# Kernel optimization log

Measured on AMD Instinct MI355X. Metric: run time of the kernel, lower is better.

The kernel has to match this reference:

```python
import jax, jax.numpy as jnp
import numpy as np

ATT_DEPTH = 3
PATCH = 8


def setup_inputs() -> dict:
    key = jax.random.key(0)
    k1, k2 = jax.random.split(key)
    B, C, H, W = 8, 16, 512, 512
    x = jax.random.normal(k1, (B, C, H, W), dtype=jnp.float32)
    L = (H // PATCH) * (W // PATCH)            # 4096 target patches
    Lp = (H // (PATCH * 2 ** ATT_DEPTH)) * (W // (PATCH * 2 ** ATT_DEPTH))  # 64 source patches
    attentions = jax.random.uniform(k2, (B, 1, L, Lp), dtype=jnp.float32)
    return {"x": x, "attentions": attentions}


def reference(x, attentions):
    B, C, H, W = x.shape
    d = 2 ** ATT_DEPTH
    p = PATCH
    # depthwise ones-conv stride d, divided by d*d == average pooling
    argx = x.reshape(B, C, H // d, d, W // d, d).mean(axis=(3, 5))  # [B,C,h,w]
    h, w = H // d, W // d
    hp, wp = h // p, w // p
    # nn.Unfold(kernel=p, stride=p): channels ordered (C, kh, kw), locations row-major
    unf = (argx.reshape(B, C, hp, p, wp, p)
               .transpose(0, 1, 3, 5, 2, 4)
               .reshape(B, C * p * p, hp * wp))  # [B, C*p*p, L']
    # normalize attention rows by nonzero count (non-differentiable int count)
    nz = jax.lax.stop_gradient(
        jnp.count_nonzero(attentions, axis=-1).astype(attentions.dtype)
    )[..., None] + 1e-05  # [B,1,L,1]
    # [B,1,L,L'] @ [B,1,L',C*p*p] -> [B,1,L,C*p*p]
    att = jnp.matmul(attentions / nz, unf[:, None].transpose(0, 1, 3, 2))
    att = jnp.squeeze(att, axis=1).transpose(0, 2, 1)  # [B, C*p*p, L]
    # Fold(output=(H,W), kernel=p, stride=p): non-overlapping -> pure reshape
    Hp, Wp = H // p, W // p
    out = (att.reshape(B, C, p, p, Hp, Wp)
              .transpose(0, 1, 4, 2, 5, 3)
              .reshape(B, C, H, W))
    return out
```

## Files before the change

kernel.cpp:

```cpp
#include <hip/hip_runtime.h>
#include <hip/hip_bf16.h>

typedef __attribute__((ext_vector_type(4))) float f32x4;
typedef __attribute__((ext_vector_type(8))) short s16x8;

#define NB 8
#define NC 16
#define HH 512
#define WW 512

__global__ __launch_bounds__(256) void pool_to_bt(const float* __restrict__ x,
                                                  __hip_bfloat16* __restrict__ bt) {
    int flat = blockIdx.x * 256 + threadIdx.x;
    int wq = flat & 63;
    int hq = (flat >> 6) & 63;
    int c  = (flat >> 12) & 15;
    int b  = flat >> 16;
    const float* base = x + ((size_t)(b * NC + c) * HH + hq * 8) * WW + wq * 8;
    float s = 0.f;
#pragma unroll
    for (int r = 0; r < 8; ++r) {
        f32x4 v0 = *(const f32x4*)(base + (size_t)r * WW);
        f32x4 v1 = *(const f32x4*)(base + (size_t)r * WW + 4);
        s += v0[0] + v0[1] + v0[2] + v0[3] + v1[0] + v1[1] + v1[2] + v1[3];
    }
    s *= (1.f / 64.f);
    int m  = c * 64 + (hq & 7) * 8 + (wq & 7);
    int lp = (hq >> 3) * 8 + (wq >> 3);
    bt[((size_t)b * 1024 + m) * 64 + lp] = __float2bfloat16(s);
}

#define BM 128
#define BN 128
#define LDK 72

__global__ __launch_bounds__(256) void gemm_scatter(const float* __restrict__ attn,
                                                    const __hip_bfloat16* __restrict__ bt,
                                                    float* __restrict__ out) {
    int mb = blockIdx.x;
    int lb = blockIdx.y;
    int b  = blockIdx.z;

    __shared__ __align__(16) unsigned short As[BM][LDK];
    __shared__ __align__(16) unsigned short Bs[BN][LDK];

    int tid = threadIdx.x;

    {
        int row  = tid >> 1;
        int half = tid & 1;
        const float* Arow = attn + ((size_t)(b * 4096 + lb * BM + row)) * 64 + half * 32;
        f32x4 v[8];
        int cnt = 0;
#pragma unroll
        for (int j = 0; j < 8; ++j) {
            v[j] = *(const f32x4*)(Arow + j * 4);
            cnt += (v[j][0] != 0.f) + (v[j][1] != 0.f) + (v[j][2] != 0.f) + (v[j][3] != 0.f);
        }
        cnt += __shfl_xor(cnt, 1);
        float inv = 1.0f / ((float)cnt + 1e-5f);
#pragma unroll
        for (int j = 0; j < 4; ++j) {
            s16x8 o;
#pragma unroll
            for (int e = 0; e < 8; ++e) {
                __hip_bfloat16 h = __float2bfloat16(v[j * 2 + (e >> 2)][e & 3] * inv);
                o[e] = (short)*reinterpret_cast<unsigned short*>(&h);
            }
            *(s16x8*)&As[row][half * 32 + j * 8] = o;
        }
    }
    {
        const unsigned short* Bg = (const unsigned short*)bt + ((size_t)b * 1024 + mb * BN) * 64;
#pragma unroll
        for (int i = 0; i < 4; ++i) {
            int cid = tid + i * 256;
            int row = cid >> 3, c8 = cid & 7;
            *(s16x8*)&Bs[row][c8 * 8] = *(const s16x8*)(Bg + row * 64 + c8 * 8);
        }
    }
    __syncthreads();

    int w    = tid >> 6;
    int lane = tid & 63;
    int wm   = (w & 1) * 64;
    int wl   = (w >> 1) * 64;
    int lr   = lane & 15;
    int kq   = lane >> 4;

    f32x4 acc[4][4] = {};
#pragma unroll
    for (int ks = 0; ks < 2; ++ks) {
        s16x8 mf[4], lf[4];
#pragma unroll
        for (int i = 0; i < 4; ++i)
            mf[i] = *(const s16x8*)&Bs[wm + i * 16 + lr][ks * 32 + kq * 8];
#pragma unroll
        for (int j = 0; j < 4; ++j)
            lf[j] = *(const s16x8*)&As[wl + j * 16 + lr][ks * 32 + kq * 8];
#pragma unroll
        for (int i = 0; i < 4; ++i)
#pragma unroll
            for (int j = 0; j < 4; ++j)
                acc[i][j] = __builtin_amdgcn_mfma_f32_16x16x32_bf16(mf[i], lf[j], acc[i][j], 0, 0, 0);
    }

#pragma unroll
    for (int mi = 0; mi < 4; ++mi) {
        int m0 = mb * BN + wm + mi * 16 + kq * 4;
        int c  = m0 >> 6, kh = (m0 >> 3) & 7, kw = m0 & 7;
        float* obase = out + (((size_t)(b * NC + c) * HH) + kh) * WW + kw;
#pragma unroll
        for (int lj = 0; lj < 4; ++lj) {
            int l  = lb * BM + wl + lj * 16 + lr;
            int Hp = l >> 6, Wp = l & 63;
            *(f32x4*)(obase + ((size_t)Hp * 8) * WW + Wp * 8) = acc[mi][lj];
        }
    }
}

extern "C" void kernel_launch(void* const* d_in, const int* in_sizes, int n_in,
                              void* d_out, int out_size, void* d_ws, size_t ws_size,
                              hipStream_t stream) {
    const float* x    = (const float*)d_in[0];
    const float* attn = (const float*)d_in[1];
    float* out        = (float*)d_out;

    __hip_bfloat16* bt = (__hip_bfloat16*)d_ws;

    pool_to_bt<<<2048, 256, 0, stream>>>(x, bt);
    dim3 grid(8, 32, 8);
    gemm_scatter<<<grid, 256, 0, stream>>>(attn, bt, out);
}
```

Before: 56.75 us.

## Use nontemporal loads/stores, coalesce attention loads, and remap gemm block order

Loads of x in the pooling kernel and output stores in the gemm kernel become nontemporal, so streaming data bypasses cache retention. The attention tile load is restructured so 16 consecutive threads read one 64-float row with coalesced 16-byte accesses, and the nonzero count is reduced with four xor shuffles. The grid becomes 1D with batch as the fastest index and the M-block as the slowest, which changes which blocks run concurrently and how they share cache. The trade-off is more shuffle instructions per row and narrower 8-byte LDS writes.

```diff
diff --git a/kernel.cpp b/kernel.cpp
--- a/kernel.cpp
+++ b/kernel.cpp
@@ -2,6 +2,7 @@
 #include <hip/hip_bf16.h>
 
 typedef __attribute__((ext_vector_type(4))) float f32x4;
+typedef __attribute__((ext_vector_type(4))) short s16x4;
 typedef __attribute__((ext_vector_type(8))) short s16x8;
 
 #define NB 8
@@ -20,8 +21,8 @@
     float s = 0.f;
 #pragma unroll
     for (int r = 0; r < 8; ++r) {
-        f32x4 v0 = *(const f32x4*)(base + (size_t)r * WW);
-        f32x4 v1 = *(const f32x4*)(base + (size_t)r * WW + 4);
+        f32x4 v0 = __builtin_nontemporal_load((const f32x4*)(base + (size_t)r * WW));
+        f32x4 v1 = __builtin_nontemporal_load((const f32x4*)(base + (size_t)r * WW + 4));
         s += v0[0] + v0[1] + v0[2] + v0[3] + v1[0] + v1[1] + v1[2] + v1[3];
     }
     s *= (1.f / 64.f);
@@ -37,9 +38,10 @@
 __global__ __launch_bounds__(256) void gemm_scatter(const float* __restrict__ attn,
                                                     const __hip_bfloat16* __restrict__ bt,
                                                     float* __restrict__ out) {
-    int mb = blockIdx.x;
-    int lb = blockIdx.y;
-    int b  = blockIdx.z;
+    int bi = blockIdx.x;
+    int mb = bi >> 8;
+    int lb = (bi >> 3) & 31;
+    int b  = bi & 7;
 
     __shared__ __align__(16) unsigned short As[BM][LDK];
     __shared__ __align__(16) unsigned short Bs[BN][LDK];
@@ -47,27 +49,26 @@
     int tid = threadIdx.x;
 
     {
-        int row  = tid >> 1;
-        int half = tid & 1;
-        const float* Arow = attn + ((size_t)(b * 4096 + lb * BM + row)) * 64 + half * 32;
-        f32x4 v[8];
-        int cnt = 0;
+        const float* Abase = attn + ((size_t)(b * 4096 + lb * BM)) * 64;
 #pragma unroll
-        for (int j = 0; j < 8; ++j) {
-            v[j] = *(const f32x4*)(Arow + j * 4);
-            cnt += (v[j][0] != 0.f) + (v[j][1] != 0.f) + (v[j][2] != 0.f) + (v[j][3] != 0.f);
-        }
-        cnt += __shfl_xor(cnt, 1);
-        float inv = 1.0f / ((float)cnt + 1e-5f);
+        for (int i = 0; i < 8; ++i) {
+            int cid   = tid + i * 256;
+            int chunk = cid & 15;
+            int row   = cid >> 4;
+            f32x4 v = *(const f32x4*)(Abase + (size_t)row * 64 + chunk * 4);
+            int cnt = (v[0] != 0.f) + (v[1] != 0.f) + (v[2] != 0.f) + (v[3] != 0.f);
+            cnt += __shfl_xor(cnt, 1);
+            cnt += __shfl_xor(cnt, 2);
+            cnt += __shfl_xor(cnt, 4);
+            cnt += __shfl_xor(cnt, 8);
+            float inv = 1.0f / ((float)cnt + 1e-5f);
+            s16x4 o;
 #pragma unroll
-        for (int j = 0; j < 4; ++j) {
-            s16x8 o;
-#pragma unroll
-            for (int e = 0; e < 8; ++e) {
-                __hip_bfloat16 h = __float2bfloat16(v[j * 2 + (e >> 2)][e & 3] * inv);
+            for (int e = 0; e < 4; ++e) {
+                __hip_bfloat16 h = __float2bfloat16(v[e] * inv);
                 o[e] = (short)*reinterpret_cast<unsigned short*>(&h);
             }
-            *(s16x8*)&As[row][half * 32 + j * 8] = o;
+            *(s16x4*)&As[row][chunk * 4] = o;
         }
     }
     {
@@ -114,7 +115,8 @@
         for (int lj = 0; lj < 4; ++lj) {
             int l  = lb * BM + wl + lj * 16 + lr;
             int Hp = l >> 6, Wp = l & 63;
-            *(f32x4*)(obase + ((size_t)Hp * 8) * WW + Wp * 8) = acc[mi][lj];
+            __builtin_nontemporal_store(acc[mi][lj],
+                                        (f32x4*)(obase + ((size_t)Hp * 8) * WW + Wp * 8));
         }
     }
 }
@@ -129,6 +131,5 @@
     __hip_bfloat16* bt = (__hip_bfloat16*)d_ws;
 
     pool_to_bt<<<2048, 256, 0, stream>>>(x, bt);
-    dim3 grid(8, 32, 8);
-    gemm_scatter<<<grid, 256, 0, stream>>>(attn, bt, out);
+    gemm_scatter<<<2048, 256, 0, stream>>>(attn, bt, out);
 }
```

New measurement: 58.40 us. +2.9%, slower.

## Load GEMM fragments directly from global into registers, dropping LDS staging

Applied to the files above, without the earlier changes.

The GEMM kernel no longer stages A and B tiles through shared memory. Each wave loads its MFMA fragments straight from global memory, and the A rows are normalized in registers using a cross-lane shuffle count. This removes the LDS writes, LDS reads and the block barrier, and launch bounds now ask for 3 blocks per CU. In exchange each wave reloads data its sibling waves also fetch, which doubles redundant global and L2 traffic for A and B, and the per-lane global reads are strided.

```diff
diff --git a/kernel.cpp b/kernel.cpp
--- a/kernel.cpp
+++ b/kernel.cpp
@@ -30,57 +30,14 @@
     bt[((size_t)b * 1024 + m) * 64 + lp] = __float2bfloat16(s);
 }
 
-#define BM 128
-#define BN 128
-#define LDK 72
-
-__global__ __launch_bounds__(256) void gemm_scatter(const float* __restrict__ attn,
-                                                    const __hip_bfloat16* __restrict__ bt,
-                                                    float* __restrict__ out) {
+__global__ __launch_bounds__(256, 3) void gemm_scatter(const float* __restrict__ attn,
+                                                       const __hip_bfloat16* __restrict__ bt,
+                                                       float* __restrict__ out) {
     int mb = blockIdx.x;
     int lb = blockIdx.y;
     int b  = blockIdx.z;
 
-    __shared__ __align__(16) unsigned short As[BM][LDK];
-    __shared__ __align__(16) unsigned short Bs[BN][LDK];
-
-    int tid = threadIdx.x;
-
-    {
-        int row  = tid >> 1;
-        int half = tid & 1;
-        const float* Arow = attn + ((size_t)(b * 4096 + lb * BM + row)) * 64 + half * 32;
-        f32x4 v[8];
-        int cnt = 0;
-#pragma unroll
-        for (int j = 0; j < 8; ++j) {
-            v[j] = *(const f32x4*)(Arow + j * 4);
-            cnt += (v[j][0] != 0.f) + (v[j][1] != 0.f) + (v[j][2] != 0.f) + (v[j][3] != 0.f);
-        }
-        cnt += __shfl_xor(cnt, 1);
-        float inv = 1.0f / ((float)cnt + 1e-5f);
-#pragma unroll
-        for (int j = 0; j < 4; ++j) {
-            s16x8 o;
-#pragma unroll
-            for (int e = 0; e < 8; ++e) {
-                __hip_bfloat16 h = __float2bfloat16(v[j * 2 + (e >> 2)][e & 3] * inv);
-                o[e] = (short)*reinterpret_cast<unsigned short*>(&h);
-            }
-            *(s16x8*)&As[row][half * 32 + j * 8] = o;
-        }
-    }
-    {
-        const unsigned short* Bg = (const unsigned short*)bt + ((size_t)b * 1024 + mb * BN) * 64;
-#pragma unroll
-        for (int i = 0; i < 4; ++i) {
-            int cid = tid + i * 256;
-            int row = cid >> 3, c8 = cid & 7;
-            *(s16x8*)&Bs[row][c8 * 8] = *(const s16x8*)(Bg + row * 64 + c8 * 8);
-        }
-    }
-    __syncthreads();
-
+    int tid  = threadIdx.x;
     int w    = tid >> 6;
     int lane = tid & 63;
     int wm   = (w & 1) * 64;
@@ -88,31 +45,65 @@
     int lr   = lane & 15;
     int kq   = lane >> 4;
 
+    const unsigned short* Bg = (const unsigned short*)bt
+        + ((size_t)b * 1024 + mb * 128 + wm + lr) * 64 + kq * 8;
+    s16x8 mf[4][2];
+#pragma unroll
+    for (int i = 0; i < 4; ++i)
+#pragma unroll
+        for (int ks = 0; ks < 2; ++ks)
+            mf[i][ks] = *(const s16x8*)(Bg + (size_t)(i * 16) * 64 + ks * 32);
+
+    const float* Ag = attn + ((size_t)(b * 4096 + lb * 128 + wl + lr)) * 64 + kq * 8;
+    s16x8 lf[4][2];
+#pragma unroll
+    for (int j = 0; j < 4; ++j) {
+        f32x4 v[2][2];
+#pragma unroll
+        for (int ks = 0; ks < 2; ++ks) {
+            v[ks][0] = *(const f32x4*)(Ag + (size_t)(j * 16) * 64 + ks * 32);
+            v[ks][1] = *(const f32x4*)(Ag + (size_t)(j * 16) * 64 + ks * 32 + 4);
+        }
+        int cnt = 0;
+#pragma unroll
+        for (int ks = 0; ks < 2; ++ks)
+#pragma unroll
+            for (int h = 0; h < 2; ++h)
+                cnt += (v[ks][h][0] != 0.f) + (v[ks][h][1] != 0.f) +
+                       (v[ks][h][2] != 0.f) + (v[ks][h][3] != 0.f);
+        cnt += __shfl_xor(cnt, 16);
+        cnt += __shfl_xor(cnt, 32);
+        float inv = 1.0f / ((float)cnt + 1e-5f);
+#pragma unroll
+        for (int ks = 0; ks < 2; ++ks) {
+            s16x8 o;
+#pragma unroll
+            for (int e = 0; e < 8; ++e) {
+                __hip_bfloat16 h = __float2bfloat16(v[ks][e >> 2][e & 3] * inv);
+                o[e] = (short)*reinterpret_cast<unsigned short*>(&h);
+            }
+            lf[j][ks] = o;
+        }
+    }
+
     f32x4 acc[4][4] = {};
 #pragma unroll
-    for (int ks = 0; ks < 2; ++ks) {
-        s16x8 mf[4], lf[4];
-#pragma unroll
-        for (int i = 0; i < 4; ++i)
-            mf[i] = *(const s16x8*)&Bs[wm + i * 16 + lr][ks * 32 + kq * 8];
-#pragma unroll
-        for (int j = 0; j < 4; ++j)
-            lf[j] = *(const s16x8*)&As[wl + j * 16 + lr][ks * 32 + kq * 8];
+    for (int ks = 0; ks < 2; ++ks)
 #pragma unroll
         for (int i = 0; i < 4; ++i)
 #pragma unroll
             for (int j = 0; j < 4; ++j)
-                acc[i][j] = __builtin_amdgcn_mfma_f32_16x16x32_bf16(mf[i], lf[j], acc[i][j], 0, 0, 0);
-    }
+                acc[i][j] = __builtin_amdgcn_mfma_f32_16x16x32_bf16(mf[i][ks], lf[j][ks],
+                                                                    acc[i][j], 0, 0, 0);
 
 #pragma unroll
     for (int mi = 0; mi < 4; ++mi) {
-        int m0 = mb * BN + wm + mi * 16 + kq * 4;
+        int m0 = mb * 128 + wm + mi * 16 + kq * 4;
         int c  = m0 >> 6, kh = (m0 >> 3) & 7, kw = m0 & 7;
         float* obase = out + (((size_t)(b * NC + c) * HH) + kh) * WW + kw;
 #pragma unroll
         for (int lj = 0; lj < 4; ++lj) {
-            int l  = lb * BM + wl + lj * 16 + lr;
+            int l  = lb * 128 + wl + lj * 16 + lr;
             int Hp = l >> 6, Wp = l & 63;
             *(f32x4*)(obase + ((size_t)Hp * 8) * WW + Wp * 8) = acc[mi][lj];
         }
```

New measurement: 63.59 us. +12.1%, slower.

## Load B tile via global_load_lds with XOR-swizzled unpadded LDS layout

Applied to the files above, without the earlier changes.

Replaces the padded LDS tiles with unpadded 64-wide rows using an XOR swizzle on 16-byte chunks to avoid bank conflicts. The B tile now goes straight from global memory to LDS through global_load_lds instead of passing through registers. The B load is issued before the A conversion so the two overlap, and launch bounds request 5 blocks per CU. The aim is to cut LDS footprint and register traffic so occupancy can rise. The cost is more complex swizzle indexing that must match between writes and MFMA fragment reads.

```diff
diff --git a/kernel.cpp b/kernel.cpp
--- a/kernel.cpp
+++ b/kernel.cpp
@@ -30,26 +30,35 @@
     bt[((size_t)b * 1024 + m) * 64 + lp] = __float2bfloat16(s);
 }
 
-#define BM 128
-#define BN 128
-#define LDK 72
-
-__global__ __launch_bounds__(256) void gemm_scatter(const float* __restrict__ attn,
-                                                    const __hip_bfloat16* __restrict__ bt,
-                                                    float* __restrict__ out) {
+__global__ __launch_bounds__(256, 5) void gemm_scatter(const float* __restrict__ attn,
+                                                       const __hip_bfloat16* __restrict__ bt,
+                                                       float* __restrict__ out) {
     int mb = blockIdx.x;
     int lb = blockIdx.y;
     int b  = blockIdx.z;
 
-    __shared__ __align__(16) unsigned short As[BM][LDK];
-    __shared__ __align__(16) unsigned short Bs[BN][LDK];
+    __shared__ __align__(16) unsigned short As[128][64];
+    __shared__ __align__(16) unsigned short Bs[128][64];
 
     int tid = threadIdx.x;
 
     {
+        const unsigned short* Bg = (const unsigned short*)bt + ((size_t)b * 1024 + mb * 128) * 64;
+#pragma unroll
+        for (int i = 0; i < 4; ++i) {
+            int cid = tid + i * 256;
+            int row = cid >> 3, p = cid & 7;
+            const unsigned short* gsrc = Bg + row * 64 + (p ^ (row & 7)) * 8;
+            __builtin_amdgcn_global_load_lds(
+                (const __attribute__((address_space(1))) void*)gsrc,
+                (__attribute__((address_space(3))) void*)(&Bs[0][0] + (size_t)cid * 8),
+                16, 0, 0);
+        }
+    }
+    {
         int row  = tid >> 1;
         int half = tid & 1;
-        const float* Arow = attn + ((size_t)(b * 4096 + lb * BM + row)) * 64 + half * 32;
+        const float* Arow = attn + ((size_t)(b * 4096 + lb * 128 + row)) * 64 + half * 32;
         f32x4 v[8];
         int cnt = 0;
 #pragma unroll
@@ -67,16 +76,8 @@
                 __hip_bfloat16 h = __float2bfloat16(v[j * 2 + (e >> 2)][e & 3] * inv);
                 o[e] = (short)*reinterpret_cast<unsigned short*>(&h);
             }
-            *(s16x8*)&As[row][half * 32 + j * 8] = o;
-        }
-    }
-    {
-        const unsigned short* Bg = (const unsigned short*)bt + ((size_t)b * 1024 + mb * BN) * 64;
-#pragma unroll
-        for (int i = 0; i < 4; ++i) {
-            int cid = tid + i * 256;
-            int row = cid >> 3, c8 = cid & 7;
-            *(s16x8*)&Bs[row][c8 * 8] = *(const s16x8*)(Bg + row * 64 + c8 * 8);
+            int p = (half * 4 + j) ^ (row & 7);
+            *(s16x8*)&As[row][p * 8] = o;
         }
     }
     __syncthreads();
@@ -87,17 +88,19 @@
     int wl   = (w >> 1) * 64;
     int lr   = lane & 15;
     int kq   = lane >> 4;
+    int sw   = lr & 7;
 
     f32x4 acc[4][4] = {};
 #pragma unroll
     for (int ks = 0; ks < 2; ++ks) {
+        int p = (ks * 4 + kq) ^ sw;
         s16x8 mf[4], lf[4];
 #pragma unroll
         for (int i = 0; i < 4; ++i)
-            mf[i] = *(const s16x8*)&Bs[wm + i * 16 + lr][ks * 32 + kq * 8];
+            mf[i] = *(const s16x8*)&Bs[wm + i * 16 + lr][p * 8];
 #pragma unroll
         for (int j = 0; j < 4; ++j)
-            lf[j] = *(const s16x8*)&As[wl + j * 16 + lr][ks * 32 + kq * 8];
+            lf[j] = *(const s16x8*)&As[wl + j * 16 + lr][p * 8];
 #pragma unroll
         for (int i = 0; i < 4; ++i)
 #pragma unroll
@@ -107,12 +110,12 @@
 
 #pragma unroll
     for (int mi = 0; mi < 4; ++mi) {
-        int m0 = mb * BN + wm + mi * 16 + kq * 4;
+        int m0 = mb * 128 + wm + mi * 16 + kq * 4;
         int c  = m0 >> 6, kh = (m0 >> 3) & 7, kw = m0 & 7;
         float* obase = out + (((size_t)(b * NC + c) * HH) + kh) * WW + kw;
 #pragma unroll
         for (int lj = 0; lj < 4; ++lj) {
-            int l  = lb * BM + wl + lj * 16 + lr;
+            int l  = lb * 128 + wl + lj * 16 + lr;
             int Hp = l >> 6, Wp = l & 63;
             *(f32x4*)(obase + ((size_t)Hp * 8) * WW + Wp * 8) = acc[mi][lj];
         }
```

Result: no change. 56.20 us (-1.0%).
